# Performance work log

Hardware: AMD Instinct MI355X
Metric: run time of the kernel (lower is better)

## Reference

```python
import jax, jax.numpy as jnp
import numpy as np

D_MODEL = 1024
NHEAD = 16
D_FF = 4096
SEQ = 2048
BATCH = 2
EPS = 1e-5


def _layernorm(x, g, b):
    mu = jnp.mean(x, axis=-1, keepdims=True)
    var = jnp.var(x, axis=-1, keepdims=True)
    return (x - mu) * jax.lax.rsqrt(var + EPS) * g + b


def setup_inputs() -> dict:
    key = jax.random.key(0)
    ks = jax.random.split(key, 16)
    s = 0.02
    def lin(k, din, dout):
        return jax.random.normal(k, (din, dout), jnp.float32) * s
    return {
        "x": jax.random.normal(ks[0], (SEQ, BATCH, D_MODEL), jnp.float32),
        "Wq": lin(ks[1], D_MODEL, D_MODEL), "bq": jnp.zeros((D_MODEL,), jnp.float32),
        "Wk": lin(ks[2], D_MODEL, D_MODEL), "bk": jnp.zeros((D_MODEL,), jnp.float32),
        "Wv": lin(ks[3], D_MODEL, D_MODEL), "bv": jnp.zeros((D_MODEL,), jnp.float32),
        "Wo": lin(ks[4], D_MODEL, D_MODEL), "bo": jnp.zeros((D_MODEL,), jnp.float32),
        "W1": lin(ks[5], D_MODEL, D_FF), "b1": jnp.zeros((D_FF,), jnp.float32),
        "W2": lin(ks[6], D_FF, D_MODEL), "b2": jnp.zeros((D_MODEL,), jnp.float32),
        "g1": jnp.ones((D_MODEL,), jnp.float32), "be1": jnp.zeros((D_MODEL,), jnp.float32),
        "g2": jnp.ones((D_MODEL,), jnp.float32), "be2": jnp.zeros((D_MODEL,), jnp.float32),
    }


def reference(x, Wq, bq, Wk, bk, Wv, bv, Wo, bo, W1, b1, W2, b2, g1, be1, g2, be2):
    # batch_first=False: x is [S, B, D] -> [B, S, D]
    xb = jnp.transpose(x, (1, 0, 2))
    B, S, D = xb.shape
    H, Dh = NHEAD, D // NHEAD

    Q = (xb @ Wq + bq).reshape(B, S, H, Dh)
    K = (xb @ Wk + bk).reshape(B, S, H, Dh)
    V = (xb @ Wv + bv).reshape(B, S, H, Dh)

    scores = jnp.einsum('bqhd,bkhd->bhqk', Q, K) / jnp.sqrt(jnp.float32(Dh))
    attn = jax.nn.softmax(scores, axis=-1)
    ctx = jnp.einsum('bhqk,bkhd->bqhd', attn, V).reshape(B, S, D)

    x_att = ctx @ Wo + bo
    xb = xb + x_att
    xb = _layernorm(xb, g1, be1)  # post-norm (norm_first=False)

    h = jax.nn.gelu(xb @ W1 + b1, approximate=False)
    xb = xb + (h @ W2 + b2)
    xb = _layernorm(xb, g2, be2)

    return jnp.transpose(xb, (1, 0, 2))  # back to [S, B, D]
```

## Files before the change

kernel.cpp:

```cpp
#include <hip/hip_runtime.h>
#include <hip/hip_bf16.h>
#include <cstdint>
#include <cstddef>

#define S_LEN 2048
#define BATCHN 2
#define DMODEL 1024
#define NHEADS 16
#define DHEAD 64
#define DFF 4096
#define NTOK (S_LEN*BATCHN)

typedef __bf16 bf16x8 __attribute__((ext_vector_type(8)));
typedef __bf16 bf16x4 __attribute__((ext_vector_type(4)));
typedef float f32x4 __attribute__((ext_vector_type(4)));
typedef __hip_bfloat16 bf16s;

#define QSCALE 0.18033688011112042592f

__device__ static inline void gload_lds16(const void* g, void* l) {
  __builtin_amdgcn_global_load_lds((const __attribute__((address_space(1))) void*)g,
                                   (__attribute__((address_space(3))) void*)l,
                                   16, 0, 0);
}


__global__ __launch_bounds__(256) void transpose_convert(const float* __restrict__ in,
                                                         bf16s* __restrict__ out,
                                                         int K, int N) {
  __shared__ float tile[32][33];
  const int tx = threadIdx.x & 31;
  const int ty = threadIdx.x >> 5;
  const int bx = blockIdx.x * 32;
  const int by = blockIdx.y * 32;
#pragma unroll
  for (int i = 0; i < 32; i += 8)
    tile[ty + i][tx] = in[(size_t)(by + ty + i) * N + bx + tx];
  __syncthreads();
#pragma unroll
  for (int i = 0; i < 32; i += 8)
    out[(size_t)(bx + ty + i) * K + by + tx] = __float2bfloat16(tile[tx][ty + i]);
}

__global__ __launch_bounds__(256) void cvt_bf16_kernel(const float* __restrict__ in,
                                                       bf16s* __restrict__ out, int n4) {
  int i = blockIdx.x * 256 + threadIdx.x;
  if (i < n4) {
    float4 v = ((const float4*)in)[i];
    union { bf16s h[4]; uint2 u; } pk;
    pk.h[0] = __float2bfloat16(v.x); pk.h[1] = __float2bfloat16(v.y);
    pk.h[2] = __float2bfloat16(v.z); pk.h[3] = __float2bfloat16(v.w);
    ((uint2*)out)[i] = pk.u;
  }
}

__global__ __launch_bounds__(256) void bias_concat_kernel(const float* __restrict__ bq,
                                                          const float* __restrict__ bk,
                                                          const float* __restrict__ bv,
                                                          float* __restrict__ bqkv) {
  int i = blockIdx.x * 256 + threadIdx.x;
  if (i < 3 * DMODEL) {
    float v = (i < DMODEL) ? bq[i] : (i < 2 * DMODEL ? bk[i - DMODEL] : bv[i - 2 * DMODEL]);
    bqkv[i] = v;
  }
}

template<int EPI>
__global__ __launch_bounds__(256, 2)
void gemm_kernel(const bf16s* __restrict__ A, const bf16s* __restrict__ Bt,
                 int M, int N, int K,
                 const float* __restrict__ bias,
                 const float* __restrict__ residF,
                 const bf16s* __restrict__ residB,
                 float* __restrict__ outF, bf16s* __restrict__ outB,
                 bf16s* __restrict__ Qb, bf16s* __restrict__ Kb, bf16s* __restrict__ Vtb)
{
  __shared__ bf16s smem[2][2 * 128 * 64];
  const int tid = threadIdx.x;
  const int l = tid & 63;
  const int w = tid >> 6;
  const int m0 = blockIdx.y * 128;
  const int n0 = blockIdx.x * 128;
  const int lr = l & 15, lg = l >> 4;

  f32x4 acc[4][4] = {};

  auto stageAB = [&](int buf, int kt) {
#pragma unroll
    for (int it = 0; it < 4; ++it) {
      int c = it * 4 + w;
      int off = c * 1024 + l * 16;
      int row = off >> 7;
      int kb = (off & 127) ^ ((row & 7) << 4);
      const char* srcA = (const char*)A + ((size_t)(m0 + row) * K + kt) * 2 + kb;
      gload_lds16(srcA, (char*)&smem[buf][0] + c * 1024);
      const char* srcB = (const char*)Bt + ((size_t)(n0 + row) * K + kt) * 2 + kb;
      gload_lds16(srcB, (char*)&smem[buf][0] + 16384 + c * 1024);
    }
  };

  auto compute = [&](int buf) {
    const char* base = (const char*)&smem[buf][0];
    const int wm = (w >> 1) * 64, wn = (w & 1) * 64;
#pragma unroll
    for (int kk = 0; kk < 2; ++kk) {
      bf16x8 af[4], bfr[4];
#pragma unroll
      for (int mi = 0; mi < 4; ++mi) {
        int row = wm + mi * 16 + lr;
        int kb = (kk * 64 + lg * 16) ^ ((row & 7) << 4);
        af[mi] = *(const bf16x8*)(base + row * 128 + kb);
      }
#pragma unroll
      for (int ni = 0; ni < 4; ++ni) {
        int row = wn + ni * 16 + lr;
        int kb = (kk * 64 + lg * 16) ^ ((row & 7) << 4);
        bfr[ni] = *(const bf16x8*)(base + 16384 + row * 128 + kb);
      }
#pragma unroll
      for (int mi = 0; mi < 4; ++mi)
#pragma unroll
        for (int ni = 0; ni < 4; ++ni)
          acc[mi][ni] = __builtin_amdgcn_mfma_f32_16x16x32_bf16(af[mi], bfr[ni], acc[mi][ni], 0, 0, 0);
    }
  };

  const int nt = K / 64;
  stageAB(0, 0);
  __syncthreads();
  int cur = 0;
  for (int t = 0; t < nt - 1; ++t) {
    stageAB(cur ^ 1, (t + 1) * 64);
    compute(cur);
    __syncthreads();
    cur ^= 1;
  }
  compute(cur);

  const int wm = (w >> 1) * 64, wn = (w & 1) * 64;
#pragma unroll
  for (int mi = 0; mi < 4; ++mi) {
#pragma unroll
    for (int ni = 0; ni < 4; ++ni) {
#pragma unroll
      for (int r = 0; r < 4; ++r) {
        int row = m0 + wm + mi * 16 + lg * 4 + r;
        int col = n0 + wn + ni * 16 + lr;
        float v = acc[mi][ni][r] + bias[col];
        if (EPI == 0) {
          int which = col >> 10;
          int h = (col & 1023) >> 6;
          int d = col & 63;
          int b = row & 1;
          int s = row >> 1;
          if (which == 0)
            Qb[(((size_t)(b * NHEADS + h)) * S_LEN + s) * DHEAD + d] = __float2bfloat16(v * QSCALE);
          else if (which == 1)
            Kb[(((size_t)(b * NHEADS + h)) * S_LEN + s) * DHEAD + d] = __float2bfloat16(v);
          else
            Vtb[(((size_t)(b * NHEADS + h)) * DHEAD + d) * S_LEN + s] = __float2bfloat16(v);
        } else if (EPI == 1) {
          outF[(size_t)row * N + col] = v + residF[(size_t)row * N + col];
        } else if (EPI == 2) {
          float gv = 0.5f * v * (1.0f + erff(v * 0.70710678118654752f));
          outB[(size_t)row * N + col] = __float2bfloat16(gv);
        } else {
          outF[(size_t)row * N + col] = v + __bfloat162float(residB[(size_t)row * N + col]);
        }
      }
    }
  }
}

__global__ __launch_bounds__(256, 2)
void attn_kernel(const bf16s* __restrict__ Qb, const bf16s* __restrict__ Kb,
                 const bf16s* __restrict__ Vtb, bf16s* __restrict__ ctx)
{
  __shared__ __align__(1024) char lds[51200];
  const int tid = threadIdx.x;
  const int l = tid & 63, w = tid >> 6;
  const int lr = l & 15, lg = l >> 4;

  int lin = blockIdx.x;
  int wg = (lin & 7) * 64 + (lin >> 3);
  int qb = wg & 15;
  int hb = wg >> 4;
  int h = hb & 15, b = hb >> 4;

  const char* Qg = (const char*)(Qb + ((size_t)(b * NHEADS + h)) * S_LEN * DHEAD);
  const char* Kg = (const char*)(Kb + ((size_t)(b * NHEADS + h)) * S_LEN * DHEAD);
  const char* Vg = (const char*)(Vtb + ((size_t)(b * NHEADS + h)) * DHEAD * S_LEN);

  const int swz = (lr & 7) << 4;
  const int aK0 = lr * 128 + ((lg * 16) ^ swz);
  const int aK1 = lr * 128 + ((64 + lg * 16) ^ swz);
  const int klane = (l >> 3) * 128  + (((l & 7) * 16) ^ ((l & 56) << 1));
  const int vlane = (l >> 3) * 4096 + (((l & 7) * 16) ^ ((l & 56) << 1));
  const int l16 = l * 16;
  char* Pw = lds + 32768 + w * 4608;
  const int pwA = lr * 144 + lg * 8;
  const int prA = lr * 144 + lg * 16;

  const int q0 = qb * 128 + w * 32;
  bf16x8 aq[2][2];
#pragma unroll
  for (int qi = 0; qi < 2; ++qi)
#pragma unroll
    for (int kk = 0; kk < 2; ++kk)
      aq[qi][kk] = *(const bf16x8*)(Qg + (size_t)(q0 + qi * 16 + lr) * 128 + kk * 64 + lg * 16);

  f32x4 o0[4] = {}, o1[4] = {};
  float m0 = -1e30f, m1 = -1e30f;
  float ls0 = 0.f, ls1 = 0.f;

  const int NT = S_LEN / 64;

  auto stage = [&](char* dK, int tile) {
    const char* kbg = Kg + (size_t)tile * 8192;
    const char* vbg = Vg + (size_t)tile * 128;
    char* dV = dK + 8192;
#pragma unroll
    for (int i = 0; i < 2; ++i) {
      int c = w * 2 + i;
      gload_lds16(kbg + c * 1024 + klane, dK + c * 1024 + l16);
      gload_lds16(vbg + (size_t)c * 32768 + vlane, dV + c * 1024 + l16);
    }
  };

  stage(lds, 0);
  asm volatile("s_waitcnt vmcnt(0)" ::: "memory");
  __builtin_amdgcn_s_barrier();

#define ATTN_ITER(BUF, t)                                                        \
  {                                                                              \
    int nxt = ((t) + 1 < NT) ? (t) + 1 : NT - 1;                                 \
    stage(lds + ((BUF) ^ 1) * 16384, nxt);                                       \
    const char* bK = lds + (BUF) * 16384;                                        \
    const char* bV = bK + 8192;                                                  \
    f32x4 st0[4], st1[4];                                                        \
    _Pragma("unroll")                                                            \
    for (int ni = 0; ni < 4; ++ni) {                                             \
      bf16x8 k0 = *(const bf16x8*)(bK + ni * 2048 + aK0);                        \
      bf16x8 k1 = *(const bf16x8*)(bK + ni * 2048 + aK1);                        \
      f32x4 z = {};                                                              \
      st0[ni] = __builtin_amdgcn_mfma_f32_16x16x32_bf16(k0, aq[0][0], z, 0, 0, 0);\
      st0[ni] = __builtin_amdgcn_mfma_f32_16x16x32_bf16(k1, aq[0][1], st0[ni], 0, 0, 0);\
      st1[ni] = __builtin_amdgcn_mfma_f32_16x16x32_bf16(k0, aq[1][0], z, 0, 0, 0);\
      st1[ni] = __builtin_amdgcn_mfma_f32_16x16x32_bf16(k1, aq[1][1], st1[ni], 0, 0, 0);\
    }                                                                            \
    f32x4 vm0 = st0[0], vm1 = st1[0];                                            \
    _Pragma("unroll")                                                            \
    for (int ni = 1; ni < 4; ++ni) {                                             \
      _Pragma("unroll")                                                          \
      for (int r = 0; r < 4; ++r) {                                              \
        vm0[r] = fmaxf(vm0[r], st0[ni][r]);                                      \
        vm1[r] = fmaxf(vm1[r], st1[ni][r]);                                      \
      }                                                                          \
    }                                                                            \
    float mx0 = fmaxf(fmaxf(vm0[0], vm0[1]), fmaxf(vm0[2], vm0[3]));             \
    float mx1 = fmaxf(fmaxf(vm1[0], vm1[1]), fmaxf(vm1[2], vm1[3]));             \
    mx0 = fmaxf(mx0, __shfl_xor(mx0, 16)); mx0 = fmaxf(mx0, __shfl_xor(mx0, 32));\
    mx1 = fmaxf(mx1, __shfl_xor(mx1, 16)); mx1 = fmaxf(mx1, __shfl_xor(mx1, 32));\
    if (!__all(mx0 <= m0 + 8.f && mx1 <= m1 + 8.f)) {                            \
      float nm0 = fmaxf(m0, mx0), nm1 = fmaxf(m1, mx1);                          \
      float al0 = exp2f(m0 - nm0), al1 = exp2f(m1 - nm1);                        \
      m0 = nm0; m1 = nm1; ls0 *= al0; ls1 *= al1;                                \
      _Pragma("unroll")                                                          \
      for (int r = 0; r < 4; ++r) {                                              \
        float s0r = __shfl(al0, lg * 4 + r);                                     \
        float s1r = __shfl(al1, lg * 4 + r);                                     \
        _Pragma("unroll")                                                        \
        for (int di = 0; di < 4; ++di) { o0[di][r] *= s0r; o1[di][r] *= s1r; }   \
      }                                                                          \
    }                                                                            \
    f32x4 ac0 = {}, ac1 = {};                                                    \
    _Pragma("unroll")                                                            \
    for (int ni = 0; ni < 4; ++ni) {                                             \
      _Pragma("unroll")                                                          \
      for (int r = 0; r < 4; ++r) {                                              \
        st0[ni][r] = exp2f(st0[ni][r] - m0);                                     \
        st1[ni][r] = exp2f(st1[ni][r] - m1);                                     \
      }                                                                          \
      ac0 += st0[ni]; ac1 += st1[ni];                                            \
    }                                                                            \
    ls0 += ac0[0] + ac0[1] + ac0[2] + ac0[3];                                    \
    ls1 += ac1[0] + ac1[1] + ac1[2] + ac1[3];                                    \
    _Pragma("unroll")                                                            \
    for (int ni = 0; ni < 4; ++ni) {                                             \
      bf16x4 p0, p1;                                                             \
      _Pragma("unroll")                                                          \
      for (int j = 0; j < 4; ++j) { p0[j] = (__bf16)st0[ni][j]; p1[j] = (__bf16)st1[ni][j]; }\
      *(bf16x4*)(Pw + pwA + ni * 32) = p0;                                       \
      *(bf16x4*)(Pw + 2304 + pwA + ni * 32) = p1;                                \
    }                                                                            \
    _Pragma("unroll")                                                            \
    for (int kk = 0; kk < 2; ++kk) {                                             \
      bf16x8 ap0 = *(const bf16x8*)(Pw + prA + kk * 64);                         \
      bf16x8 ap1 = *(const bf16x8*)(Pw + 2304 + prA + kk * 64);                  \
      const int av = kk ? aK1 : aK0;                                             \
      _Pragma("unroll")                                                          \
      for (int di = 0; di < 4; ++di) {                                           \
        bf16x8 vv = *(const bf16x8*)(bV + di * 2048 + av);                       \
        o0[di] = __builtin_amdgcn_mfma_f32_16x16x32_bf16(ap0, vv, o0[di], 0, 0, 0);\
        o1[di] = __builtin_amdgcn_mfma_f32_16x16x32_bf16(ap1, vv, o1[di], 0, 0, 0);\
      }                                                                          \
    }                                                                            \
    asm volatile("s_waitcnt vmcnt(0)" ::: "memory");                             \
    __builtin_amdgcn_s_barrier();                                                \
  }

  for (int t = 0; t < NT; t += 2) {
    ATTN_ITER(0, t);
    ATTN_ITER(1, t + 1);
  }
#undef ATTN_ITER

#pragma unroll
  for (int qi = 0; qi < 2; ++qi) {
    float ls = qi ? ls1 : ls0;
    ls += __shfl_xor(ls, 16);
    ls += __shfl_xor(ls, 32);
    float inv = 1.0f / ls;
#pragma unroll
    for (int r = 0; r < 4; ++r) {
      float invr = __shfl(inv, lg * 4 + r);
      int srow = q0 + qi * 16 + lg * 4 + r;
      int tkn = srow * BATCHN + b;
#pragma unroll
      for (int di = 0; di < 4; ++di) {
        int d = h * DHEAD + di * 16 + lr;
        float v = (qi ? o1[di][r] : o0[di][r]) * invr;
        ctx[(size_t)tkn * DMODEL + d] = __float2bfloat16(v);
      }
    }
  }
}

template<int OUTBF>
__global__ __launch_bounds__(256)
void ln_kernel(const float* __restrict__ in, const float* __restrict__ g,
               const float* __restrict__ be, float* __restrict__ outF,
               bf16s* __restrict__ outB)
{
  const int row = blockIdx.x;
  const int tid = threadIdx.x;
  const float* x = in + (size_t)row * DMODEL;
  float4 v = ((const float4*)x)[tid];
  float s = v.x + v.y + v.z + v.w;
  float s2 = v.x * v.x + v.y * v.y + v.z * v.z + v.w * v.w;
#pragma unroll
  for (int m = 1; m < 64; m <<= 1) { s += __shfl_xor(s, m); s2 += __shfl_xor(s2, m); }
  __shared__ float sm[8];
  const int wv = tid >> 6, l = tid & 63;
  if (l == 0) { sm[wv] = s; sm[4 + wv] = s2; }
  __syncthreads();
  s = sm[0] + sm[1] + sm[2] + sm[3];
  s2 = sm[4] + sm[5] + sm[6] + sm[7];
  float mean = s * (1.0f / DMODEL);
  float var = s2 * (1.0f / DMODEL) - mean * mean;
  float rstd = rsqrtf(var + 1e-5f);
  float4 gv = ((const float4*)g)[tid];
  float4 bv = ((const float4*)be)[tid];
  float o0 = (v.x - mean) * rstd * gv.x + bv.x;
  float o1 = (v.y - mean) * rstd * gv.y + bv.y;
  float o2 = (v.z - mean) * rstd * gv.z + bv.z;
  float o3 = (v.w - mean) * rstd * gv.w + bv.w;
  if (OUTBF) {
    union { bf16s h[4]; uint2 u; } pk;
    pk.h[0] = __float2bfloat16(o0); pk.h[1] = __float2bfloat16(o1);
    pk.h[2] = __float2bfloat16(o2); pk.h[3] = __float2bfloat16(o3);
    ((uint2*)(outB + (size_t)row * DMODEL))[tid] = pk.u;
  } else {
    float4 ov = {o0, o1, o2, o3};
    ((float4*)(outF + (size_t)row * DMODEL))[tid] = ov;
  }
}

extern "C" void kernel_launch(void* const* d_in, const int* in_sizes, int n_in,
                              void* d_out, int out_size, void* d_ws, size_t ws_size,
                              hipStream_t stream) {
  const float* x  = (const float*)d_in[0];
  const float* Wq = (const float*)d_in[1];
  const float* bq = (const float*)d_in[2];
  const float* Wk = (const float*)d_in[3];
  const float* bk = (const float*)d_in[4];
  const float* Wv = (const float*)d_in[5];
  const float* bv = (const float*)d_in[6];
  const float* Wo = (const float*)d_in[7];
  const float* bo = (const float*)d_in[8];
  const float* W1 = (const float*)d_in[9];
  const float* b1 = (const float*)d_in[10];
  const float* W2 = (const float*)d_in[11];
  const float* b2 = (const float*)d_in[12];
  const float* g1 = (const float*)d_in[13];
  const float* be1 = (const float*)d_in[14];
  const float* g2 = (const float*)d_in[15];
  const float* be2 = (const float*)d_in[16];

  char* ws = (char*)d_ws;
  size_t off = 0;
  auto alloc = [&](size_t bytes) -> void* {
    void* p = ws + off;
    off += (bytes + 255) & ~(size_t)255;
    return p;
  };
  bf16s* Wqkv_t = (bf16s*)alloc((size_t)3 * DMODEL * DMODEL * 2);
  bf16s* Wo_t   = (bf16s*)alloc((size_t)DMODEL * DMODEL * 2);
  bf16s* W1_t   = (bf16s*)alloc((size_t)DFF * DMODEL * 2);
  bf16s* W2_t   = (bf16s*)alloc((size_t)DMODEL * DFF * 2);
  float* bqkv   = (float*)alloc((size_t)3 * DMODEL * 4);
  bf16s* Xb     = (bf16s*)alloc((size_t)NTOK * DMODEL * 2);
  bf16s* Qb     = (bf16s*)alloc((size_t)NTOK * DMODEL * 2);
  bf16s* Kb     = (bf16s*)alloc((size_t)NTOK * DMODEL * 2);
  bf16s* Vtb    = (bf16s*)alloc((size_t)NTOK * DMODEL * 2);
  bf16s* ctx    = (bf16s*)alloc((size_t)NTOK * DMODEL * 2);
  float* s1     = (float*)alloc((size_t)NTOK * DMODEL * 4);
  bf16s* y1     = (bf16s*)alloc((size_t)NTOK * DMODEL * 2);
  bf16s* Hb     = (bf16s*)alloc((size_t)NTOK * DFF * 2);
  if (off > ws_size) return;

  transpose_convert<<<dim3(DMODEL / 32, DMODEL / 32), 256, 0, stream>>>(Wq, Wqkv_t, DMODEL, DMODEL);
  transpose_convert<<<dim3(DMODEL / 32, DMODEL / 32), 256, 0, stream>>>(Wk, Wqkv_t + (size_t)DMODEL * DMODEL, DMODEL, DMODEL);
  transpose_convert<<<dim3(DMODEL / 32, DMODEL / 32), 256, 0, stream>>>(Wv, Wqkv_t + (size_t)2 * DMODEL * DMODEL, DMODEL, DMODEL);
  transpose_convert<<<dim3(DMODEL / 32, DMODEL / 32), 256, 0, stream>>>(Wo, Wo_t, DMODEL, DMODEL);
  transpose_convert<<<dim3(DFF / 32, DMODEL / 32), 256, 0, stream>>>(W1, W1_t, DMODEL, DFF);
  transpose_convert<<<dim3(DMODEL / 32, DFF / 32), 256, 0, stream>>>(W2, W2_t, DFF, DMODEL);
  bias_concat_kernel<<<12, 256, 0, stream>>>(bq, bk, bv, bqkv);
  cvt_bf16_kernel<<<(NTOK * DMODEL / 4 + 255) / 256, 256, 0, stream>>>(x, Xb, NTOK * DMODEL / 4);

  gemm_kernel<0><<<dim3(3 * DMODEL / 128, NTOK / 128), 256, 0, stream>>>(
      Xb, Wqkv_t, NTOK, 3 * DMODEL, DMODEL, bqkv, nullptr, nullptr, nullptr, nullptr, Qb, Kb, Vtb);

  attn_kernel<<<512, 256, 0, stream>>>(Qb, Kb, Vtb, ctx);

  gemm_kernel<1><<<dim3(DMODEL / 128, NTOK / 128), 256, 0, stream>>>(
      ctx, Wo_t, NTOK, DMODEL, DMODEL, bo, x, nullptr, s1, nullptr, nullptr, nullptr, nullptr);
  ln_kernel<1><<<NTOK, 256, 0, stream>>>(s1, g1, be1, nullptr, y1);
  gemm_kernel<2><<<dim3(DFF / 128, NTOK / 128), 256, 0, stream>>>(
      y1, W1_t, NTOK, DFF, DMODEL, b1, nullptr, nullptr, nullptr, Hb, nullptr, nullptr, nullptr);
  gemm_kernel<3><<<dim3(DMODEL / 128, NTOK / 128), 256, 0, stream>>>(
      Hb, W2_t, NTOK, DMODEL, DFF, b2, nullptr, y1, s1, nullptr, nullptr, nullptr, nullptr);
  ln_kernel<0><<<NTOK, 256, 0, stream>>>(s1, g2, be2, (float*)d_out, nullptr);
}
```

Before: 396.8 us.

## Add 256x256 GEMM tiles with triple-buffered pipeline and batch weight transposes

Adds a 512-thread GEMM with 256x256 tiles for the QKV and FFN1 projections, and reworks the 128x128 GEMM used for the output and FFN2 projections. Both use K-step 32 with a three-stage LDS ring, explicit vmcnt waits and a single barrier per step. This raises data reuse per tile and overlaps loads with MFMA work. The four square weight transposes are merged into one launch. Larger tiles mean fewer blocks for the QKV GEMM (192 blocks) and more register pressure, which could hurt occupancy.

```diff
diff --git a/kernel.cpp b/kernel.cpp
--- a/kernel.cpp
+++ b/kernel.cpp
@@ -24,6 +24,27 @@
                                    16, 0, 0);
 }
 
+
+__global__ __launch_bounds__(256) void transpose_convert4(const float* __restrict__ s0,
+                                                          const float* __restrict__ s1,
+                                                          const float* __restrict__ s2,
+                                                          const float* __restrict__ s3,
+                                                          bf16s* __restrict__ dst) {
+  __shared__ float tile[32][33];
+  const float* in = (blockIdx.z == 0) ? s0 : (blockIdx.z == 1) ? s1 : (blockIdx.z == 2) ? s2 : s3;
+  bf16s* out = dst + (size_t)blockIdx.z * DMODEL * DMODEL;
+  const int tx = threadIdx.x & 31;
+  const int ty = threadIdx.x >> 5;
+  const int bx = blockIdx.x * 32;
+  const int by = blockIdx.y * 32;
+#pragma unroll
+  for (int i = 0; i < 32; i += 8)
+    tile[ty + i][tx] = in[(size_t)(by + ty + i) * DMODEL + bx + tx];
+  __syncthreads();
+#pragma unroll
+  for (int i = 0; i < 32; i += 8)
+    out[(size_t)(bx + ty + i) * DMODEL + by + tx] = __float2bfloat16(tile[tx][ty + i]);
+}
 
 __global__ __launch_bounds__(256) void transpose_convert(const float* __restrict__ in,
                                                          bf16s* __restrict__ out,
@@ -66,110 +87,211 @@
 }
 
 template<int EPI>
-__global__ __launch_bounds__(256, 2)
-void gemm_kernel(const bf16s* __restrict__ A, const bf16s* __restrict__ Bt,
-                 int M, int N, int K,
-                 const float* __restrict__ bias,
-                 const float* __restrict__ residF,
-                 const bf16s* __restrict__ residB,
-                 float* __restrict__ outF, bf16s* __restrict__ outB,
-                 bf16s* __restrict__ Qb, bf16s* __restrict__ Kb, bf16s* __restrict__ Vtb)
+__device__ static inline void epi_store(int row, int col, int N, float v,
+                                        const float* __restrict__ residF,
+                                        const bf16s* __restrict__ residB,
+                                        float* __restrict__ outF, bf16s* __restrict__ outB,
+                                        bf16s* __restrict__ Qb, bf16s* __restrict__ Kb,
+                                        bf16s* __restrict__ Vtb) {
+  if (EPI == 0) {
+    int which = col >> 10;
+    int h = (col & 1023) >> 6;
+    int d = col & 63;
+    int b = row & 1;
+    int s = row >> 1;
+    if (which == 0)
+      Qb[(((size_t)(b * NHEADS + h)) * S_LEN + s) * DHEAD + d] = __float2bfloat16(v * QSCALE);
+    else if (which == 1)
+      Kb[(((size_t)(b * NHEADS + h)) * S_LEN + s) * DHEAD + d] = __float2bfloat16(v);
+    else
+      Vtb[(((size_t)(b * NHEADS + h)) * DHEAD + d) * S_LEN + s] = __float2bfloat16(v);
+  } else if (EPI == 1) {
+    outF[(size_t)row * N + col] = v + residF[(size_t)row * N + col];
+  } else if (EPI == 2) {
+    float gv = 0.5f * v * (1.0f + erff(v * 0.70710678118654752f));
+    outB[(size_t)row * N + col] = __float2bfloat16(gv);
+  } else {
+    outF[(size_t)row * N + col] = v + __bfloat162float(residB[(size_t)row * N + col]);
+  }
+}
+
+template<int EPI>
+__global__ __launch_bounds__(512, 2)
+void gemm256_kernel(const bf16s* __restrict__ A, const bf16s* __restrict__ Bt,
+                    int M, int N, int K,
+                    const float* __restrict__ bias,
+                    const float* __restrict__ residF,
+                    const bf16s* __restrict__ residB,
+                    float* __restrict__ outF, bf16s* __restrict__ outB,
+                    bf16s* __restrict__ Qb, bf16s* __restrict__ Kb, bf16s* __restrict__ Vtb)
 {
-  __shared__ bf16s smem[2][2 * 128 * 64];
+  __shared__ __align__(1024) char smem[3 * 32768];
   const int tid = threadIdx.x;
-  const int l = tid & 63;
-  const int w = tid >> 6;
+  const int l = tid & 63, w = tid >> 6;
+  const int m0 = blockIdx.y * 256;
+  const int n0 = blockIdx.x * 256;
+  const int lr = l & 15, lg = l >> 4;
+  const int wmB = (w >> 2) * 128, wnB = (w & 3) * 64;
+
+  f32x4 acc[8][4] = {};
+
+  auto stage = [&](int buf, int kt) {
+    char* base = smem + buf * 32768;
+#pragma unroll
+    for (int c = 0; c < 2; ++c) {
+      int off = c * 8192 + tid * 16;
+      int row = off >> 6;
+      int kb = (off & 63) ^ ((row & 3) << 4);
+      gload_lds16((const char*)A + ((size_t)(m0 + row) * K + kt * 32) * 2 + kb, base + off);
+    }
+#pragma unroll
+    for (int c = 0; c < 2; ++c) {
+      int off = c * 8192 + tid * 16;
+      int row = off >> 6;
+      int kb = (off & 63) ^ ((row & 3) << 4);
+      gload_lds16((const char*)Bt + ((size_t)(n0 + row) * K + kt * 32) * 2 + kb, base + 16384 + off);
+    }
+  };
+
+  auto compute = [&](int buf) {
+    const char* base = smem + buf * 32768;
+    bf16x8 bfr[4];
+#pragma unroll
+    for (int ni = 0; ni < 4; ++ni) {
+      int row = wnB + ni * 16 + lr;
+      bfr[ni] = *(const bf16x8*)(base + 16384 + row * 64 + ((lg * 16) ^ ((row & 3) << 4)));
+    }
+#pragma unroll
+    for (int mi = 0; mi < 8; ++mi) {
+      int row = wmB + mi * 16 + lr;
+      bf16x8 af = *(const bf16x8*)(base + row * 64 + ((lg * 16) ^ ((row & 3) << 4)));
+#pragma unroll
+      for (int ni = 0; ni < 4; ++ni)
+        acc[mi][ni] = __builtin_amdgcn_mfma_f32_16x16x32_bf16(af, bfr[ni], acc[mi][ni], 0, 0, 0);
+    }
+  };
+
+  const int nt = K / 32;
+  stage(0, 0);
+  stage(1, 1);
+  int cur = 0;
+  for (int t = 0; t < nt - 1; ++t) {
+    asm volatile("s_waitcnt vmcnt(4)" ::: "memory");
+    __builtin_amdgcn_s_barrier();
+    __builtin_amdgcn_sched_barrier(0);
+    if (t + 2 < nt) {
+      int sb = cur + 2; if (sb >= 3) sb -= 3;
+      stage(sb, t + 2);
+    }
+    compute(cur);
+    if (++cur == 3) cur = 0;
+  }
+  asm volatile("s_waitcnt vmcnt(0)" ::: "memory");
+  __builtin_amdgcn_s_barrier();
+  __builtin_amdgcn_sched_barrier(0);
+  compute(cur);
+
+#pragma unroll
+  for (int mi = 0; mi < 8; ++mi)
+#pragma unroll
+    for (int ni = 0; ni < 4; ++ni)
+#pragma unroll
+      for (int r = 0; r < 4; ++r) {
+        int row = m0 + wmB + mi * 16 + lg * 4 + r;
+        int col = n0 + wnB + ni * 16 + lr;
+        epi_store<EPI>(row, col, N, acc[mi][ni][r] + bias[col],
+                       residF, residB, outF, outB, Qb, Kb, Vtb);
+      }
+}
+
+template<int EPI>
+__global__ __launch_bounds__(256, 3)
+void gemm128_kernel(const bf16s* __restrict__ A, const bf16s* __restrict__ Bt,
+                    int M, int N, int K,
+                    const float* __restrict__ bias,
+                    const float* __restrict__ residF,
+                    const bf16s* __restrict__ residB,
+                    float* __restrict__ outF, bf16s* __restrict__ outB)
+{
+  __shared__ __align__(1024) char smem[3 * 16384];
+  const int tid = threadIdx.x;
+  const int l = tid & 63, w = tid >> 6;
   const int m0 = blockIdx.y * 128;
   const int n0 = blockIdx.x * 128;
   const int lr = l & 15, lg = l >> 4;
+  const int wm = (w >> 1) * 64, wn = (w & 1) * 64;
 
   f32x4 acc[4][4] = {};
 
-  auto stageAB = [&](int buf, int kt) {
-#pragma unroll
-    for (int it = 0; it < 4; ++it) {
-      int c = it * 4 + w;
-      int off = c * 1024 + l * 16;
-      int row = off >> 7;
-      int kb = (off & 127) ^ ((row & 7) << 4);
-      const char* srcA = (const char*)A + ((size_t)(m0 + row) * K + kt) * 2 + kb;
-      gload_lds16(srcA, (char*)&smem[buf][0] + c * 1024);
-      const char* srcB = (const char*)Bt + ((size_t)(n0 + row) * K + kt) * 2 + kb;
-      gload_lds16(srcB, (char*)&smem[buf][0] + 16384 + c * 1024);
+  auto stage = [&](int buf, int kt) {
+    char* base = smem + buf * 16384;
+#pragma unroll
+    for (int c = 0; c < 2; ++c) {
+      int off = c * 4096 + tid * 16;
+      int row = off >> 6;
+      int kb = (off & 63) ^ ((row & 3) << 4);
+      gload_lds16((const char*)A + ((size_t)(m0 + row) * K + kt * 32) * 2 + kb, base + off);
+    }
+#pragma unroll
+    for (int c = 0; c < 2; ++c) {
+      int off = c * 4096 + tid * 16;
+      int row = off >> 6;
+      int kb = (off & 63) ^ ((row & 3) << 4);
+      gload_lds16((const char*)Bt + ((size_t)(n0 + row) * K + kt * 32) * 2 + kb, base + 8192 + off);
     }
   };
 
   auto compute = [&](int buf) {
-    const char* base = (const char*)&smem[buf][0];
-    const int wm = (w >> 1) * 64, wn = (w & 1) * 64;
-#pragma unroll
-    for (int kk = 0; kk < 2; ++kk) {
-      bf16x8 af[4], bfr[4];
-#pragma unroll
-      for (int mi = 0; mi < 4; ++mi) {
-        int row = wm + mi * 16 + lr;
-        int kb = (kk * 64 + lg * 16) ^ ((row & 7) << 4);
-        af[mi] = *(const bf16x8*)(base + row * 128 + kb);
-      }
-#pragma unroll
-      for (int ni = 0; ni < 4; ++ni) {
-        int row = wn + ni * 16 + lr;
-        int kb = (kk * 64 + lg * 16) ^ ((row & 7) << 4);
-        bfr[ni] = *(const bf16x8*)(base + 16384 + row * 128 + kb);
-      }
-#pragma unroll
-      for (int mi = 0; mi < 4; ++mi)
-#pragma unroll
-        for (int ni = 0; ni < 4; ++ni)
-          acc[mi][ni] = __builtin_amdgcn_mfma_f32_16x16x32_bf16(af[mi], bfr[ni], acc[mi][ni], 0, 0, 0);
-    }
+    const char* base = smem + buf * 16384;
+    bf16x8 af[4], bfr[4];
+#pragma unroll
+    for (int mi = 0; mi < 4; ++mi) {
+      int row = wm + mi * 16 + lr;
+      af[mi] = *(const bf16x8*)(base + row * 64 + ((lg * 16) ^ ((row & 3) << 4)));
+    }
+#pragma unroll
+    for (int ni = 0; ni < 4; ++ni) {
+      int row = wn + ni * 16 + lr;
+      bfr[ni] = *(const bf16x8*)(base + 8192 + row * 64 + ((lg * 16) ^ ((row & 3) << 4)));
+    }
+#pragma unroll
+    for (int mi = 0; mi < 4; ++mi)
+#pragma unroll
+      for (int ni = 0; ni < 4; ++ni)
+        acc[mi][ni] = __builtin_amdgcn_mfma_f32_16x16x32_bf16(af[mi], bfr[ni], acc[mi][ni], 0, 0, 0);
   };
 
-  const int nt = K / 64;
-  stageAB(0, 0);
-  __syncthreads();
+  const int nt = K / 32;
+  stage(0, 0);
+  stage(1, 1);
   int cur = 0;
   for (int t = 0; t < nt - 1; ++t) {
-    stageAB(cur ^ 1, (t + 1) * 64);
+    asm volatile("s_waitcnt vmcnt(4)" ::: "memory");
+    __builtin_amdgcn_s_barrier();
+    __builtin_amdgcn_sched_barrier(0);
+    if (t + 2 < nt) {
+      int sb = cur + 2; if (sb >= 3) sb -= 3;
+      stage(sb, t + 2);
+    }
     compute(cur);
-    __syncthreads();
-    cur ^= 1;
-  }
+    if (++cur == 3) cur = 0;
+  }
+  asm volatile("s_waitcnt vmcnt(0)" ::: "memory");
+  __builtin_amdgcn_s_barrier();
+  __builtin_amdgcn_sched_barrier(0);
   compute(cur);
 
-  const int wm = (w >> 1) * 64, wn = (w & 1) * 64;
-#pragma unroll
-  for (int mi = 0; mi < 4; ++mi) {
-#pragma unroll
-    for (int ni = 0; ni < 4; ++ni) {
+#pragma unroll
+  for (int mi = 0; mi < 4; ++mi)
+#pragma unroll
+    for (int ni = 0; ni < 4; ++ni)
 #pragma unroll
       for (int r = 0; r < 4; ++r) {
         int row = m0 + wm + mi * 16 + lg * 4 + r;
         int col = n0 + wn + ni * 16 + lr;
-        float v = acc[mi][ni][r] + bias[col];
-        if (EPI == 0) {
-          int which = col >> 10;
-          int h = (col & 1023) >> 6;
-          int d = col & 63;
-          int b = row & 1;
-          int s = row >> 1;
-          if (which == 0)
-            Qb[(((size_t)(b * NHEADS + h)) * S_LEN + s) * DHEAD + d] = __float2bfloat16(v * QSCALE);
-          else if (which == 1)
-            Kb[(((size_t)(b * NHEADS + h)) * S_LEN + s) * DHEAD + d] = __float2bfloat16(v);
-          else
-            Vtb[(((size_t)(b * NHEADS + h)) * DHEAD + d) * S_LEN + s] = __float2bfloat16(v);
-        } else if (EPI == 1) {
-          outF[(size_t)row * N + col] = v + residF[(size_t)row * N + col];
-        } else if (EPI == 2) {
-          float gv = 0.5f * v * (1.0f + erff(v * 0.70710678118654752f));
-          outB[(size_t)row * N + col] = __float2bfloat16(gv);
-        } else {
-          outF[(size_t)row * N + col] = v + __bfloat162float(residB[(size_t)row * N + col]);
-        }
+        epi_store<EPI>(row, col, N, acc[mi][ni][r] + bias[col],
+                       residF, residB, outF, outB, nullptr, nullptr, nullptr);
       }
-    }
-  }
 }
 
 __global__ __launch_bounds__(256, 2)
@@ -419,26 +541,23 @@
   bf16s* Hb     = (bf16s*)alloc((size_t)NTOK * DFF * 2);
   if (off > ws_size) return;
 
-  transpose_convert<<<dim3(DMODEL / 32, DMODEL / 32), 256, 0, stream>>>(Wq, Wqkv_t, DMODEL, DMODEL);
-  transpose_convert<<<dim3(DMODEL / 32, DMODEL / 32), 256, 0, stream>>>(Wk, Wqkv_t + (size_t)DMODEL * DMODEL, DMODEL, DMODEL);
-  transpose_convert<<<dim3(DMODEL / 32, DMODEL / 32), 256, 0, stream>>>(Wv, Wqkv_t + (size_t)2 * DMODEL * DMODEL, DMODEL, DMODEL);
-  transpose_convert<<<dim3(DMODEL / 32, DMODEL / 32), 256, 0, stream>>>(Wo, Wo_t, DMODEL, DMODEL);
+  transpose_convert4<<<dim3(32, 32, 4), 256, 0, stream>>>(Wq, Wk, Wv, Wo, Wqkv_t);
   transpose_convert<<<dim3(DFF / 32, DMODEL / 32), 256, 0, stream>>>(W1, W1_t, DMODEL, DFF);
   transpose_convert<<<dim3(DMODEL / 32, DFF / 32), 256, 0, stream>>>(W2, W2_t, DFF, DMODEL);
   bias_concat_kernel<<<12, 256, 0, stream>>>(bq, bk, bv, bqkv);
   cvt_bf16_kernel<<<(NTOK * DMODEL / 4 + 255) / 256, 256, 0, stream>>>(x, Xb, NTOK * DMODEL / 4);
 
-  gemm_kernel<0><<<dim3(3 * DMODEL / 128, NTOK / 128), 256, 0, stream>>>(
+  gemm256_kernel<0><<<dim3(3 * DMODEL / 256, NTOK / 256), 512, 0, stream>>>(
       Xb, Wqkv_t, NTOK, 3 * DMODEL, DMODEL, bqkv, nullptr, nullptr, nullptr, nullptr, Qb, Kb, Vtb);
 
   attn_kernel<<<512, 256, 0, stream>>>(Qb, Kb, Vtb, ctx);
 
-  gemm_kernel<1><<<dim3(DMODEL / 128, NTOK / 128), 256, 0, stream>>>(
-      ctx, Wo_t, NTOK, DMODEL, DMODEL, bo, x, nullptr, s1, nullptr, nullptr, nullptr, nullptr);
+  gemm128_kernel<1><<<dim3(DMODEL / 128, NTOK / 128), 256, 0, stream>>>(
+      ctx, Wo_t, NTOK, DMODEL, DMODEL, bo, x, nullptr, s1, nullptr);
   ln_kernel<1><<<NTOK, 256, 0, stream>>>(s1, g1, be1, nullptr, y1);
-  gemm_kernel<2><<<dim3(DFF / 128, NTOK / 128), 256, 0, stream>>>(
+  gemm256_kernel<2><<<dim3(DFF / 256, NTOK / 256), 512, 0, stream>>>(
       y1, W1_t, NTOK, DFF, DMODEL, b1, nullptr, nullptr, nullptr, Hb, nullptr, nullptr, nullptr);
-  gemm_kernel<3><<<dim3(DMODEL / 128, NTOK / 128), 256, 0, stream>>>(
-      Hb, W2_t, NTOK, DMODEL, DFF, b2, nullptr, y1, s1, nullptr, nullptr, nullptr, nullptr);
+  gemm128_kernel<3><<<dim3(DMODEL / 128, NTOK / 128), 256, 0, stream>>>(
+      Hb, W2_t, NTOK, DMODEL, DFF, b2, nullptr, y1, s1, nullptr);
   ln_kernel<0><<<NTOK, 256, 0, stream>>>(s1, g2, be2, (float*)d_out, nullptr);
 }
```

Result: slower. 410.2 us (+3.4%).

## Split-K the N=1024 GEMMs and fold bias and residual into layernorm

Applied to the files above, without the earlier changes.

The output-projection and W2 GEMMs are split along K into two halves, written to separate fp32 buffers, and summed with bias and residual inside the layernorm kernel. The GEMM k-tile shrinks from 64 to 32 with simplified unswizzled LDS addressing, and the occupancy hint rises to 3 blocks per CU. The four square weight transposes merge into one launch, and the FFN hidden buffer reuses the Q/K/V/ctx workspace. The aim is to fill more CUs on the small-N GEMMs and cut launches, at the cost of extra fp32 partial-sum traffic and possible LDS bank conflicts from dropping the swizzle.

```diff
diff --git a/kernel.cpp b/kernel.cpp
--- a/kernel.cpp
+++ b/kernel.cpp
@@ -24,6 +24,27 @@
                                    16, 0, 0);
 }
 
+
+__global__ __launch_bounds__(256) void transpose_convert4(const float* __restrict__ s0,
+                                                          const float* __restrict__ s1,
+                                                          const float* __restrict__ s2,
+                                                          const float* __restrict__ s3,
+                                                          bf16s* __restrict__ dst) {
+  __shared__ float tile[32][33];
+  const float* in = (blockIdx.z == 0) ? s0 : (blockIdx.z == 1) ? s1 : (blockIdx.z == 2) ? s2 : s3;
+  bf16s* out = dst + (size_t)blockIdx.z * DMODEL * DMODEL;
+  const int tx = threadIdx.x & 31;
+  const int ty = threadIdx.x >> 5;
+  const int bx = blockIdx.x * 32;
+  const int by = blockIdx.y * 32;
+#pragma unroll
+  for (int i = 0; i < 32; i += 8)
+    tile[ty + i][tx] = in[(size_t)(by + ty + i) * DMODEL + bx + tx];
+  __syncthreads();
+#pragma unroll
+  for (int i = 0; i < 32; i += 8)
+    out[(size_t)(bx + ty + i) * DMODEL + by + tx] = __float2bfloat16(tile[tx][ty + i]);
+}
 
 __global__ __launch_bounds__(256) void transpose_convert(const float* __restrict__ in,
                                                          bf16s* __restrict__ out,
@@ -66,78 +87,70 @@
 }
 
 template<int EPI>
-__global__ __launch_bounds__(256, 2)
+__global__ __launch_bounds__(256, 3)
 void gemm_kernel(const bf16s* __restrict__ A, const bf16s* __restrict__ Bt,
-                 int M, int N, int K,
+                 int N, int K, int kchunk,
                  const float* __restrict__ bias,
-                 const float* __restrict__ residF,
-                 const bf16s* __restrict__ residB,
                  float* __restrict__ outF, bf16s* __restrict__ outB,
                  bf16s* __restrict__ Qb, bf16s* __restrict__ Kb, bf16s* __restrict__ Vtb)
 {
-  __shared__ bf16s smem[2][2 * 128 * 64];
+  __shared__ bf16s smem[2][8192];
   const int tid = threadIdx.x;
-  const int l = tid & 63;
-  const int w = tid >> 6;
+  const int l = tid & 63, w = tid >> 6;
   const int m0 = blockIdx.y * 128;
   const int n0 = blockIdx.x * 128;
+  const int kbeg = blockIdx.z * kchunk;
   const int lr = l & 15, lg = l >> 4;
+  const int wm = (w >> 1) * 64, wn = (w & 1) * 64;
+
+  const int off0 = (w * 2 + 0) * 1024 + l * 16;
+  const int off1 = (w * 2 + 1) * 1024 + l * 16;
+  const char* a0 = (const char*)(A + (size_t)(m0 + (off0 >> 6)) * K + kbeg) + (off0 & 63);
+  const char* a1 = (const char*)(A + (size_t)(m0 + (off1 >> 6)) * K + kbeg) + (off1 & 63);
+  const char* b0 = (const char*)(Bt + (size_t)(n0 + (off0 >> 6)) * K + kbeg) + (off0 & 63);
+  const char* b1 = (const char*)(Bt + (size_t)(n0 + (off1 >> 6)) * K + kbeg) + (off1 & 63);
 
   f32x4 acc[4][4] = {};
 
-  auto stageAB = [&](int buf, int kt) {
-#pragma unroll
-    for (int it = 0; it < 4; ++it) {
-      int c = it * 4 + w;
-      int off = c * 1024 + l * 16;
-      int row = off >> 7;
-      int kb = (off & 127) ^ ((row & 7) << 4);
-      const char* srcA = (const char*)A + ((size_t)(m0 + row) * K + kt) * 2 + kb;
-      gload_lds16(srcA, (char*)&smem[buf][0] + c * 1024);
-      const char* srcB = (const char*)Bt + ((size_t)(n0 + row) * K + kt) * 2 + kb;
-      gload_lds16(srcB, (char*)&smem[buf][0] + 16384 + c * 1024);
-    }
+  auto stage = [&](int buf, int t) {
+    char* s = (char*)&smem[buf][0];
+    size_t kb = (size_t)t * 64;
+    gload_lds16(a0 + kb, s + off0);
+    gload_lds16(a1 + kb, s + off1);
+    gload_lds16(b0 + kb, s + 8192 + off0);
+    gload_lds16(b1 + kb, s + 8192 + off1);
   };
+
+  const int ao = (wm + lr) * 64 + lg * 16;
+  const int bo = 8192 + (wn + lr) * 64 + lg * 16;
 
   auto compute = [&](int buf) {
     const char* base = (const char*)&smem[buf][0];
-    const int wm = (w >> 1) * 64, wn = (w & 1) * 64;
-#pragma unroll
-    for (int kk = 0; kk < 2; ++kk) {
-      bf16x8 af[4], bfr[4];
-#pragma unroll
-      for (int mi = 0; mi < 4; ++mi) {
-        int row = wm + mi * 16 + lr;
-        int kb = (kk * 64 + lg * 16) ^ ((row & 7) << 4);
-        af[mi] = *(const bf16x8*)(base + row * 128 + kb);
-      }
-#pragma unroll
-      for (int ni = 0; ni < 4; ++ni) {
-        int row = wn + ni * 16 + lr;
-        int kb = (kk * 64 + lg * 16) ^ ((row & 7) << 4);
-        bfr[ni] = *(const bf16x8*)(base + 16384 + row * 128 + kb);
-      }
-#pragma unroll
-      for (int mi = 0; mi < 4; ++mi)
-#pragma unroll
-        for (int ni = 0; ni < 4; ++ni)
-          acc[mi][ni] = __builtin_amdgcn_mfma_f32_16x16x32_bf16(af[mi], bfr[ni], acc[mi][ni], 0, 0, 0);
-    }
+    bf16x8 af[4], bfr[4];
+#pragma unroll
+    for (int mi = 0; mi < 4; ++mi) af[mi] = *(const bf16x8*)(base + ao + mi * 1024);
+#pragma unroll
+    for (int ni = 0; ni < 4; ++ni) bfr[ni] = *(const bf16x8*)(base + bo + ni * 1024);
+#pragma unroll
+    for (int mi = 0; mi < 4; ++mi)
+#pragma unroll
+      for (int ni = 0; ni < 4; ++ni)
+        acc[mi][ni] = __builtin_amdgcn_mfma_f32_16x16x32_bf16(af[mi], bfr[ni], acc[mi][ni], 0, 0, 0);
   };
 
-  const int nt = K / 64;
-  stageAB(0, 0);
+  const int nt = kchunk / 32;
+  stage(0, 0);
   __syncthreads();
   int cur = 0;
   for (int t = 0; t < nt - 1; ++t) {
-    stageAB(cur ^ 1, (t + 1) * 64);
+    stage(cur ^ 1, t + 1);
     compute(cur);
     __syncthreads();
     cur ^= 1;
   }
   compute(cur);
 
-  const int wm = (w >> 1) * 64, wn = (w & 1) * 64;
+  float* outFz = (EPI == 1) ? outF + (size_t)blockIdx.z * ((size_t)NTOK * DMODEL) : outF;
 #pragma unroll
   for (int mi = 0; mi < 4; ++mi) {
 #pragma unroll
@@ -146,8 +159,9 @@
       for (int r = 0; r < 4; ++r) {
         int row = m0 + wm + mi * 16 + lg * 4 + r;
         int col = n0 + wn + ni * 16 + lr;
-        float v = acc[mi][ni][r] + bias[col];
+        float v = acc[mi][ni][r];
         if (EPI == 0) {
+          v += bias[col];
           int which = col >> 10;
           int h = (col & 1023) >> 6;
           int d = col & 63;
@@ -160,12 +174,11 @@
           else
             Vtb[(((size_t)(b * NHEADS + h)) * DHEAD + d) * S_LEN + s] = __float2bfloat16(v);
         } else if (EPI == 1) {
-          outF[(size_t)row * N + col] = v + residF[(size_t)row * N + col];
-        } else if (EPI == 2) {
+          outFz[(size_t)row * N + col] = v;
+        } else {
+          v += bias[col];
           float gv = 0.5f * v * (1.0f + erff(v * 0.70710678118654752f));
           outB[(size_t)row * N + col] = __float2bfloat16(gv);
-        } else {
-          outF[(size_t)row * N + col] = v + __bfloat162float(residB[(size_t)row * N + col]);
         }
       }
     }
@@ -336,16 +349,25 @@
   }
 }
 
-template<int OUTBF>
+template<int WB>
 __global__ __launch_bounds__(256)
-void ln_kernel(const float* __restrict__ in, const float* __restrict__ g,
-               const float* __restrict__ be, float* __restrict__ outF,
-               bf16s* __restrict__ outB)
+void ln_kernel(const float* __restrict__ inA, const float* __restrict__ inB,
+               const float* __restrict__ resid, const float* __restrict__ bias,
+               const float* __restrict__ g, const float* __restrict__ be,
+               float* __restrict__ outF, bf16s* __restrict__ outB)
 {
   const int row = blockIdx.x;
   const int tid = threadIdx.x;
-  const float* x = in + (size_t)row * DMODEL;
-  float4 v = ((const float4*)x)[tid];
+  const size_t base = (size_t)row * DMODEL;
+  float4 a = ((const float4*)(inA + base))[tid];
+  float4 bq = ((const float4*)(inB + base))[tid];
+  float4 rr = ((const float4*)(resid + base))[tid];
+  float4 bi = ((const float4*)bias)[tid];
+  float4 v;
+  v.x = a.x + bq.x + rr.x + bi.x;
+  v.y = a.y + bq.y + rr.y + bi.y;
+  v.z = a.z + bq.z + rr.z + bi.z;
+  v.w = a.w + bq.w + rr.w + bi.w;
   float s = v.x + v.y + v.z + v.w;
   float s2 = v.x * v.x + v.y * v.y + v.z * v.z + v.w * v.w;
 #pragma unroll
@@ -365,14 +387,13 @@
   float o1 = (v.y - mean) * rstd * gv.y + bv.y;
   float o2 = (v.z - mean) * rstd * gv.z + bv.z;
   float o3 = (v.w - mean) * rstd * gv.w + bv.w;
-  if (OUTBF) {
+  float4 ov = {o0, o1, o2, o3};
+  ((float4*)(outF + base))[tid] = ov;
+  if (WB) {
     union { bf16s h[4]; uint2 u; } pk;
     pk.h[0] = __float2bfloat16(o0); pk.h[1] = __float2bfloat16(o1);
     pk.h[2] = __float2bfloat16(o2); pk.h[3] = __float2bfloat16(o3);
-    ((uint2*)(outB + (size_t)row * DMODEL))[tid] = pk.u;
-  } else {
-    float4 ov = {o0, o1, o2, o3};
-    ((float4*)(outF + (size_t)row * DMODEL))[tid] = ov;
+    ((uint2*)(outB + base))[tid] = pk.u;
   }
 }
 
@@ -414,31 +435,32 @@
   bf16s* Kb     = (bf16s*)alloc((size_t)NTOK * DMODEL * 2);
   bf16s* Vtb    = (bf16s*)alloc((size_t)NTOK * DMODEL * 2);
   bf16s* ctx    = (bf16s*)alloc((size_t)NTOK * DMODEL * 2);
-  float* s1     = (float*)alloc((size_t)NTOK * DMODEL * 4);
+  float* sAB    = (float*)alloc((size_t)2 * NTOK * DMODEL * 4);
   bf16s* y1     = (bf16s*)alloc((size_t)NTOK * DMODEL * 2);
-  bf16s* Hb     = (bf16s*)alloc((size_t)NTOK * DFF * 2);
+  float* y1f    = (float*)alloc((size_t)NTOK * DMODEL * 4);
+  bf16s* Hb     = Qb;
   if (off > ws_size) return;
 
-  transpose_convert<<<dim3(DMODEL / 32, DMODEL / 32), 256, 0, stream>>>(Wq, Wqkv_t, DMODEL, DMODEL);
-  transpose_convert<<<dim3(DMODEL / 32, DMODEL / 32), 256, 0, stream>>>(Wk, Wqkv_t + (size_t)DMODEL * DMODEL, DMODEL, DMODEL);
-  transpose_convert<<<dim3(DMODEL / 32, DMODEL / 32), 256, 0, stream>>>(Wv, Wqkv_t + (size_t)2 * DMODEL * DMODEL, DMODEL, DMODEL);
-  transpose_convert<<<dim3(DMODEL / 32, DMODEL / 32), 256, 0, stream>>>(Wo, Wo_t, DMODEL, DMODEL);
+  float* sA = sAB;
+  float* sB = sAB + (size_t)NTOK * DMODEL;
+
+  transpose_convert4<<<dim3(32, 32, 4), 256, 0, stream>>>(Wq, Wk, Wv, Wo, Wqkv_t);
   transpose_convert<<<dim3(DFF / 32, DMODEL / 32), 256, 0, stream>>>(W1, W1_t, DMODEL, DFF);
   transpose_convert<<<dim3(DMODEL / 32, DFF / 32), 256, 0, stream>>>(W2, W2_t, DFF, DMODEL);
   bias_concat_kernel<<<12, 256, 0, stream>>>(bq, bk, bv, bqkv);
   cvt_bf16_kernel<<<(NTOK * DMODEL / 4 + 255) / 256, 256, 0, stream>>>(x, Xb, NTOK * DMODEL / 4);
 
-  gemm_kernel<0><<<dim3(3 * DMODEL / 128, NTOK / 128), 256, 0, stream>>>(
-      Xb, Wqkv_t, NTOK, 3 * DMODEL, DMODEL, bqkv, nullptr, nullptr, nullptr, nullptr, Qb, Kb, Vtb);
+  gemm_kernel<0><<<dim3(24, 32, 1), 256, 0, stream>>>(
+      Xb, Wqkv_t, 3 * DMODEL, DMODEL, DMODEL, bqkv, nullptr, nullptr, Qb, Kb, Vtb);
 
   attn_kernel<<<512, 256, 0, stream>>>(Qb, Kb, Vtb, ctx);
 
-  gemm_kernel<1><<<dim3(DMODEL / 128, NTOK / 128), 256, 0, stream>>>(
-      ctx, Wo_t, NTOK, DMODEL, DMODEL, bo, x, nullptr, s1, nullptr, nullptr, nullptr, nullptr);
-  ln_kernel<1><<<NTOK, 256, 0, stream>>>(s1, g1, be1, nullptr, y1);
-  gemm_kernel<2><<<dim3(DFF / 128, NTOK / 128), 256, 0, stream>>>(
-      y1, W1_t, NTOK, DFF, DMODEL, b1, nullptr, nullptr, nullptr, Hb, nullptr, nullptr, nullptr);
-  gemm_kernel<3><<<dim3(DMODEL / 128, NTOK / 128), 256, 0, stream>>>(
-      Hb, W2_t, NTOK, DMODEL, DFF, b2, nullptr, y1, s1, nullptr, nullptr, nullptr, nullptr);
-  ln_kernel<0><<<NTOK, 256, 0, stream>>>(s1, g2, be2, (float*)d_out, nullptr);
-}
+  gemm_kernel<1><<<dim3(8, 32, 2), 256, 0, stream>>>(
+      ctx, Wo_t, DMODEL, DMODEL, DMODEL / 2, nullptr, sAB, nullptr, nullptr, nullptr, nullptr);
+  ln_kernel<1><<<NTOK, 256, 0, stream>>>(sA, sB, x, bo, g1, be1, y1f, y1);
+  gemm_kernel<2><<<dim3(32, 32, 1), 256, 0, stream>>>(
+      y1, W1_t, DFF, DMODEL, DMODEL, b1, nullptr, Hb, nullptr, nullptr, nullptr);
+  gemm_kernel<1><<<dim3(8, 32, 2), 256, 0, stream>>>(
+      Hb, W2_t, DMODEL, DFF, DFF / 2, nullptr, sAB, nullptr, nullptr, nullptr, nullptr);
+  ln_kernel<0><<<NTOK, 256, 0, stream>>>(sA, sB, y1f, b2, g2, be2, (float*)d_out, nullptr);
+}
```

Measured after the change: 390.5 us. Within noise of the previous version (-1.6%).
